# Performance work log

Measured on AMD Instinct MI355X. Metric: run time of the kernel, lower is better.

Reference implementation:

```python
import jax, jax.numpy as jnp
import numpy as np

B, P, S, D, H, DFF, VOC = 8, 16, 512, 512, 8, 2048, 10000
DEPTH = D // H
SIGMA = 0.1
T = 256
LN_EPS = 1e-6


def setup_inputs() -> dict:
    key = jax.random.key(0)
    ks = jax.random.split(key, 40)
    n = lambda i, sh, sc=1.0: jax.random.normal(ks[i], sh, jnp.float32) * sc
    inp = {
        "r": n(0, (B, P, D)),
        "x": jax.random.randint(ks[1], (B, 1), 0, VOC),
        "K": n(2, (B, P, S, D)),
        "Vs": n(3, (B, P, S, D)),
        "w": jax.random.uniform(ks[4], (B, P, 1), jnp.float32),
        "I": jax.random.randint(ks[5], (B, P, S), 0, P),
        "t": T,
        "eps_q": n(6, (B, P, 1, D)),
        "eps_k": n(7, (B, P, 1, D)),
        "eps_v": n(8, (B, P, 1, D)),
        "eps_z": n(9, (B, P, 1, D)),
        "gumbel": -jnp.log(-jnp.log(jax.random.uniform(ks[10], (B, P, P), jnp.float32, 1e-8, 1.0))),
        "Wq": n(11, (D, D), 0.02), "bq": jnp.zeros((D,), jnp.float32),
        "Wk": n(12, (D, D), 0.02), "bk": jnp.zeros((D,), jnp.float32),
        "Wv": n(13, (D, D), 0.02), "bv": jnp.zeros((D,), jnp.float32),
        "Wo": n(14, (D, D), 0.02), "bo": jnp.zeros((D,), jnp.float32),
        "ln1_g": jnp.ones((D,), jnp.float32), "ln1_b": jnp.zeros((D,), jnp.float32),
        "ln3_g": jnp.ones((D,), jnp.float32), "ln3_b": jnp.zeros((D,), jnp.float32),
        "W1": n(15, (D, DFF), 0.02), "b1": jnp.zeros((DFF,), jnp.float32),
        "W2": n(16, (DFF, D), 0.02), "b2": jnp.zeros((D,), jnp.float32),
        "Wout": n(17, (D, VOC), 0.02), "bout": jnp.zeros((VOC,), jnp.float32),
    }
    return inp


def _layernorm(x, g, b):
    mu = jnp.mean(x, axis=-1, keepdims=True)
    var = jnp.mean((x - mu) ** 2, axis=-1, keepdims=True)
    return (x - mu) / jnp.sqrt(var + LN_EPS) * g + b


def _split_heads(x):  # (B,P,L,D) -> (B,P,H,L,depth)
    b, p, l, _ = x.shape
    return x.reshape(b, p, l, H, DEPTH).transpose(0, 1, 3, 2, 4)


def _resample(params, i_t, t):  # reorder particle axis on prefix [:t+1]
    pref = jnp.take_along_axis(params[:, :, :t + 1], i_t[:, :, None, None], axis=1)
    return jnp.concatenate([pref, params[:, :, t + 1:]], axis=2)


def reference(r, x, K, Vs, w, I, t, eps_q, eps_k, eps_v, eps_z, gumbel,
              Wq, bq, Wk, bk, Wv, bv, Wo, bo, ln1_g, ln1_b, ln3_g, ln3_b,
              W1, b1, W2, b2, Wout, bout):
    x = x.astype(jnp.int32)
    I = I.astype(jnp.int32)
    r4 = r[:, :, None, :]                                   # (B,P,1,D)
    # --- mha_smc: noisy projections + K/V buffer update at t ---
    q = r4 @ Wq + bq + SIGMA * eps_q
    k = r4 @ Wk + bk + SIGMA * eps_k
    v = r4 @ Wv + bv + SIGMA * eps_v
    K = K.at[:, :, t, :].set(k[:, :, 0, :])
    Vs = Vs.at[:, :, t, :].set(v[:, :, 0, :])
    qh = _split_heads(q)                                    # (B,P,H,1,depth)
    Kh = _split_heads(K)                                    # (B,P,H,S,depth)
    Vh = _split_heads(Vs)
    scores = jnp.einsum('bphqd,bphsd->bphqs', qh, Kh) / jnp.sqrt(jnp.float32(DEPTH))
    mask = (jnp.arange(S) <= t)[None, None, None, None, :]
    scores = jnp.where(mask, scores, jnp.float32(-1e9))
    attn = jax.nn.softmax(scores, axis=-1)                  # (B,P,H,1,S)
    zh = jnp.einsum('bphqs,bphsd->bphqd', attn, Vh)
    z = zh.transpose(0, 1, 3, 2, 4).reshape(B, P, 1, D) @ Wo + bo
    z = z + SIGMA * eps_z                                   # reparametrized output noise
    attn_weights = jnp.mean(attn, axis=2)                   # (B,P,1,S)
    # --- residual + FFN (dropout disabled: training=False) ---
    out1 = _layernorm(z + r4, ln1_g, ln1_b)
    ffn = jnp.maximum(out1 @ W1 + b1, 0.0) @ W2 + b2
    r_ = _layernorm(ffn + out1, ln3_g, ln3_b)
    predictions = r_ @ Wout + bout                          # (B,P,1,VOC)
    # --- classification importance weights ---
    probs = jax.nn.softmax(predictions, axis=-1)
    idx = jnp.broadcast_to(x.reshape(B, 1, 1, 1), (B, P, 1, 1))
    w_sq = jnp.take_along_axis(probs, idx, axis=-1)[:, :, 0, 0]  # (B,P)
    w_sq = jax.lax.stop_gradient(w_sq)
    pred2 = predictions[:, :, 0, :]                         # (B,P,VOC)
    w_for_pred = w_sq[:, :, None]
    good_avg_pred = jnp.mean(pred2, axis=1, keepdims=True)  # (B,1,VOC)
    avg_pred_after_softmax = jnp.mean(jax.nn.softmax(pred2, axis=-1), axis=1, keepdims=True)
    argmax_w = jnp.argmax(w_for_pred, axis=1)               # (B,1)
    max_prediction = jnp.take_along_axis(pred2, argmax_w[:, :, None], axis=1)  # (B,1,VOC)
    # --- sample_and_keep_indices: Gumbel-max categorical over particles ---
    logits = jnp.log(w_sq + 1e-10)                          # (B,P)
    i_t = jnp.argmax(logits[:, None, :] + gumbel, axis=-1).astype(jnp.int32)  # (B,P)
    I_pref = jnp.take_along_axis(I[:, :, :t], i_t[:, :, None], axis=1)
    I_new = jnp.concatenate([I_pref, i_t[:, :, None], I[:, :, t + 1:]], axis=2)
    # --- resampling (faithful to original: V resampled from already-resampled K) ---
    K = _resample(K, i_t, t)
    Vs = _resample(K, i_t, t)
    z = jnp.take_along_axis(z, I_new[:, :, t][:, :, None, None], axis=1)
    w_new = w_sq[:, :, None]
    return (r4, z, avg_pred_after_softmax, good_avg_pred, max_prediction,
            eps_z, attn_weights, K, Vs, w_new, I_new)
```

## Files before the change

kernel.cpp:

```cpp
#include <hip/hip_runtime.h>

#define NDFF 2048
#define NVOC 10000
#define SIGMA 0.1f

typedef float f32x4 __attribute__((ext_vector_type(4)));

#define O0 0
#define O1 65536
#define O2 131072
#define O3 211072
#define O4 291072
#define O5 371072
#define O6 436608
#define O7 502144
#define O8 34056576
#define O9 67611008
#define O10 67611136

#define WQ    0
#define WK    65536
#define WV    131072
#define WZH   196608
#define WZ    262144
#define WO1   327680
#define WH1   393216
#define WPRED 720896
#define WMAX  2000896
#define WSUM  2001024
#define WWSQ  2001152
#define WIT   2001280
#define WF2P  2001536
#define WSC   2263680

__global__ __launch_bounds__(512)
void k_qkv(const float* __restrict__ r,
           const float* __restrict__ Wq, const float* __restrict__ bq, const float* __restrict__ eq, float* __restrict__ oq,
           const float* __restrict__ Wk, const float* __restrict__ bk, const float* __restrict__ ek, float* __restrict__ ok,
           const float* __restrict__ Wv, const float* __restrict__ bv, const float* __restrict__ ev, float* __restrict__ ov)
{
    const float *W, *bias, *eps; float* out;
    if (blockIdx.z == 0)      { W = Wq; bias = bq; eps = eq; out = oq; }
    else if (blockIdx.z == 1) { W = Wk; bias = bk; eps = ek; out = ok; }
    else                      { W = Wv; bias = bv; eps = ev; out = ov; }
    int tid = threadIdx.x;
    int col = tid & 63, kq = tid >> 6;
    int colg = blockIdx.x * 64 + col;
    int row0 = blockIdx.y * 8;
    __shared__ float rs[8][512];
#pragma unroll
    for (int j = 0; j < 8; j++) rs[j][tid & 511] = r[(row0 + j) * 512 + tid];
    __syncthreads();
    float acc[8] = {0,0,0,0,0,0,0,0};
    const float* Wp = W + (kq * 64) * 512 + colg;
#pragma unroll 8
    for (int d = 0; d < 64; d++) {
        float wv = Wp[d * 512];
#pragma unroll
        for (int p = 0; p < 8; p++) acc[p] += rs[p][kq * 64 + d] * wv;
    }
    __syncthreads();
    float (*part)[8][64] = (float(*)[8][64])rs;
#pragma unroll
    for (int p = 0; p < 8; p++) part[kq][p][col] = acc[p];
    __syncthreads();
    {
        int p = tid >> 6, c = tid & 63;
        int cg = blockIdx.x * 64 + c;
        float v = 0.f;
#pragma unroll
        for (int k = 0; k < 8; k++) v += part[k][p][c];
        out[(row0 + p) * 512 + cg] = v + bias[cg] + SIGMA * eps[(row0 + p) * 512 + cg];
    }
}

__global__ __launch_bounds__(512)
void k_attn(const float* __restrict__ qws, const float* __restrict__ kws,
            const float* __restrict__ vws, const float* __restrict__ Kin,
            const float* __restrict__ Vin, const int* __restrict__ t_ptr,
            float* __restrict__ zh, float* __restrict__ scw)
{
    int t = *t_ptr;
    int bp = blockIdx.x, h = blockIdx.y;
    int tid = threadIdx.x;
    int wave = tid >> 6, lane = tid & 63;
    __shared__ float sc[512];
    __shared__ float red[8], red2[8];
    __shared__ float part[8][64];

    float4 qv = ((const float4*)(qws + bp * 512 + h * 64))[lane & 15];

    for (int sb = wave * 4; sb <= t; sb += 32) {
        int s = sb + (lane >> 4);
        bool valid = (s <= t);
        int ss = valid ? s : t;
        const float4* kr = (ss == t) ? (const float4*)(kws + bp * 512 + h * 64)
                                     : (const float4*)(Kin + (bp * 512 + ss) * 512 + h * 64);
        float4 kv = kr[lane & 15];
        float p = qv.x * kv.x + qv.y * kv.y + qv.z * kv.z + qv.w * kv.w;
#pragma unroll
        for (int m = 1; m < 16; m <<= 1) p += __shfl_xor(p, m, 64);
        if ((lane & 15) == 0 && valid) sc[s] = p * 0.125f;
    }
    __syncthreads();

    float lm = -3.0e38f;
    for (int s = tid; s <= t; s += 512) lm = fmaxf(lm, sc[s]);
#pragma unroll
    for (int o = 32; o; o >>= 1) lm = fmaxf(lm, __shfl_xor(lm, o, 64));
    if (lane == 0) red[wave] = lm;
    __syncthreads();
    float m = red[0];
#pragma unroll
    for (int i = 1; i < 8; i++) m = fmaxf(m, red[i]);
    float ls = 0.f;
    for (int s = tid; s <= t; s += 512) ls += __expf(sc[s] - m);
#pragma unroll
    for (int o = 32; o; o >>= 1) ls += __shfl_xor(ls, o, 64);
    if (lane == 0) red2[wave] = ls;
    __syncthreads();
    float tot = 0.f;
#pragma unroll
    for (int i = 0; i < 8; i++) tot += red2[i];
    float inv = 1.f / tot;
    for (int s = tid; s <= t; s += 512) {
        float a = __expf(sc[s] - m) * inv;
        sc[s] = a;
        scw[(bp * 8 + h) * 512 + s] = a;
    }
    __syncthreads();

    float acc = 0.f;
    const float* Vp = Vin + (bp * 512) * 512 + h * 64 + lane;
    int s = wave;
    for (; s + 24 < t; s += 32) {
        float v0 = __builtin_nontemporal_load(Vp + (size_t)(s     ) * 512);
        float v1 = __builtin_nontemporal_load(Vp + (size_t)(s +  8) * 512);
        float v2 = __builtin_nontemporal_load(Vp + (size_t)(s + 16) * 512);
        float v3 = __builtin_nontemporal_load(Vp + (size_t)(s + 24) * 512);
        acc += sc[s] * v0 + sc[s + 8] * v1 + sc[s + 16] * v2 + sc[s + 24] * v3;
    }
    for (; s < t; s += 8) acc += sc[s] * __builtin_nontemporal_load(Vp + (size_t)s * 512);
    if ((t & 7) == wave) acc += sc[t] * vws[bp * 512 + h * 64 + lane];
    part[wave][lane] = acc;
    __syncthreads();
    if (tid < 64) {
        float v = 0.f;
#pragma unroll
        for (int k = 0; k < 8; k++) v += part[k][tid];
        zh[bp * 512 + h * 64 + tid] = v;
    }
}

__global__ __launch_bounds__(512)
void k_zproj(const float* __restrict__ zh, const float* __restrict__ Wo,
             const float* __restrict__ bo, const float* __restrict__ epsz,
             float* __restrict__ out)
{
    int tid = threadIdx.x;
    int col = tid & 63, kq = tid >> 6;
    int colg = blockIdx.x * 64 + col;
    int row0 = blockIdx.y * 8;
    __shared__ float rs[8][512];
#pragma unroll
    for (int j = 0; j < 8; j++) rs[j][tid] = zh[(row0 + j) * 512 + tid];
    __syncthreads();
    float acc[8] = {0,0,0,0,0,0,0,0};
    const float* Wp = Wo + (kq * 64) * 512 + colg;
#pragma unroll 8
    for (int d = 0; d < 64; d++) {
        float wv = Wp[d * 512];
#pragma unroll
        for (int p = 0; p < 8; p++) acc[p] += rs[p][kq * 64 + d] * wv;
    }
    __syncthreads();
    float (*part)[8][64] = (float(*)[8][64])rs;
#pragma unroll
    for (int p = 0; p < 8; p++) part[kq][p][col] = acc[p];
    __syncthreads();
    {
        int p = tid >> 6, c = tid & 63;
        int cg = blockIdx.x * 64 + c;
        float v = 0.f;
#pragma unroll
        for (int k = 0; k < 8; k++) v += part[k][p][c];
        out[(row0 + p) * 512 + cg] = v + bo[cg] + SIGMA * epsz[(row0 + p) * 512 + cg];
    }
}

__global__ __launch_bounds__(512)
void k_ffn1(const float* __restrict__ zp, const float* __restrict__ r,
            const float* __restrict__ g, const float* __restrict__ be,
            const float* __restrict__ W1, const float* __restrict__ b1,
            float* __restrict__ o1, float* __restrict__ h1)
{
    int tid = threadIdx.x;
    int col = tid & 63, kq = tid >> 6;
    int colg = blockIdx.x * 64 + col;
    int row0 = blockIdx.y * 8;
    __shared__ float rs[8][512];
    __shared__ float sm[8], si[8];
    int wave = tid >> 6, lane = tid & 63;
#pragma unroll
    for (int j = 0; j < 8; j++) {
        int gi = (row0 + j) * 512 + tid;
        rs[j][tid] = zp[gi] + r[gi];
    }
    __syncthreads();
    {
        float s = 0.f;
        for (int c = lane; c < 512; c += 64) s += rs[wave][c];
#pragma unroll
        for (int o = 32; o; o >>= 1) s += __shfl_xor(s, o, 64);
        float mu = s * (1.f / 512.f);
        float v = 0.f;
        for (int c = lane; c < 512; c += 64) { float dx = rs[wave][c] - mu; v += dx * dx; }
#pragma unroll
        for (int o = 32; o; o >>= 1) v += __shfl_xor(v, o, 64);
        if (lane == 0) { sm[wave] = mu; si[wave] = rsqrtf(v * (1.f / 512.f) + 1e-6f); }
    }
    __syncthreads();
#pragma unroll
    for (int j = 0; j < 8; j++) {
        float val = (rs[j][tid] - sm[j]) * si[j] * g[tid] + be[tid];
        rs[j][tid] = val;
        if (blockIdx.x == 0) o1[(row0 + j) * 512 + tid] = val;
    }
    __syncthreads();
    float acc[8] = {0,0,0,0,0,0,0,0};
    const float* Wp = W1 + (kq * 64) * NDFF + colg;
#pragma unroll 8
    for (int d = 0; d < 64; d++) {
        float wv = Wp[d * NDFF];
#pragma unroll
        for (int p = 0; p < 8; p++) acc[p] += rs[p][kq * 64 + d] * wv;
    }
    __syncthreads();
    float (*part)[8][64] = (float(*)[8][64])rs;
#pragma unroll
    for (int p = 0; p < 8; p++) part[kq][p][col] = acc[p];
    __syncthreads();
    {
        int p = tid >> 6, c = tid & 63;
        int cg = blockIdx.x * 64 + c;
        float v = 0.f;
#pragma unroll
        for (int k = 0; k < 8; k++) v += part[k][p][c];
        h1[(row0 + p) * NDFF + cg] = fmaxf(v + b1[cg], 0.f);
    }
}

__global__ __launch_bounds__(512)
void k_ffn2p(const float* __restrict__ h1, const float* __restrict__ W2,
             float* __restrict__ f2p)
{
    int tid = threadIdx.x;
    int col = tid & 63, kq = tid >> 6;
    int colg = blockIdx.x * 64 + col;
    int row0 = blockIdx.y * 8;
    int ks = blockIdx.z;
    __shared__ float rs[8][512];
#pragma unroll
    for (int j = 0; j < 8; j++)
        rs[j][tid] = h1[(row0 + j) * NDFF + ks * 512 + tid];
    __syncthreads();
    float acc[8] = {0,0,0,0,0,0,0,0};
    const float* Wp = W2 + (ks * 512 + kq * 64) * 512 + colg;
#pragma unroll 8
    for (int d = 0; d < 64; d++) {
        float wv = Wp[d * 512];
#pragma unroll
        for (int p = 0; p < 8; p++) acc[p] += rs[p][kq * 64 + d] * wv;
    }
    __syncthreads();
    float (*part)[8][64] = (float(*)[8][64])rs;
#pragma unroll
    for (int p = 0; p < 8; p++) part[kq][p][col] = acc[p];
    __syncthreads();
    {
        int p = tid >> 6, c = tid & 63;
        int cg = blockIdx.x * 64 + c;
        float v = 0.f;
#pragma unroll
        for (int k = 0; k < 8; k++) v += part[k][p][c];
        f2p[ks * 65536 + (row0 + p) * 512 + cg] = v;
    }
}

__global__ __launch_bounds__(512)
void k_pred(const float* __restrict__ f2p, const float* __restrict__ b2,
            const float* __restrict__ o1, const float* __restrict__ g3,
            const float* __restrict__ b3, const float* __restrict__ Wout,
            const float* __restrict__ bout, float* __restrict__ pred)
{
    int tid = threadIdx.x;
    int col = tid & 255, kh = tid >> 8;
    int colg = blockIdx.x * 256 + col;
    int colL = min(colg, NVOC - 1);
    int row0 = blockIdx.y * 16;
    __shared__ float rs[16][512];
    __shared__ float sm[16], si[16];
    int wave = tid >> 6, lane = tid & 63;
#pragma unroll
    for (int j = 0; j < 16; j++) {
        int gi = (row0 + j) * 512 + tid;
        rs[j][tid] = f2p[gi] + f2p[65536 + gi] + f2p[131072 + gi] + f2p[196608 + gi]
                   + b2[tid] + o1[gi];
    }
    __syncthreads();
    {
        int row = wave * 2 + (lane >> 5);
        int l = lane & 31;
        float s = 0.f;
        for (int c = l; c < 512; c += 32) s += rs[row][c];
#pragma unroll
        for (int o = 16; o; o >>= 1) s += __shfl_xor(s, o, 64);
        float mu = s * (1.f / 512.f);
        float v = 0.f;
        for (int c = l; c < 512; c += 32) { float dx = rs[row][c] - mu; v += dx * dx; }
#pragma unroll
        for (int o = 16; o; o >>= 1) v += __shfl_xor(v, o, 64);
        if (l == 0) { sm[row] = mu; si[row] = rsqrtf(v * (1.f / 512.f) + 1e-6f); }
    }
    __syncthreads();
#pragma unroll
    for (int j = 0; j < 16; j++)
        rs[j][tid] = (rs[j][tid] - sm[j]) * si[j] * g3[tid] + b3[tid];
    __syncthreads();
    float acc[16];
#pragma unroll
    for (int p = 0; p < 16; p++) acc[p] = 0.f;
    const float* Wp = Wout + (kh * 256) * NVOC + colL;
#pragma unroll 4
    for (int d = 0; d < 256; d++) {
        float wv = Wp[d * NVOC];
#pragma unroll
        for (int p = 0; p < 16; p++) acc[p] += rs[p][kh * 256 + d] * wv;
    }
    __syncthreads();
    float (*part)[256] = (float(*)[256])rs;
    if (kh == 1) {
#pragma unroll
        for (int p = 0; p < 16; p++) part[p][col] = acc[p];
    }
    __syncthreads();
    if (kh == 0 && colg < NVOC) {
        float bv = bout[colg];
#pragma unroll
        for (int p = 0; p < 16; p++)
            pred[(row0 + p) * NVOC + colg] = acc[p] + part[p][col] + bv;
    }
}

__global__ __launch_bounds__(512)
void k_soft(const float* __restrict__ pred, const int* __restrict__ x,
            const float* __restrict__ scw, const int* __restrict__ t_ptr,
            float* __restrict__ rowmax, float* __restrict__ rowsum,
            float* __restrict__ wsq, float* __restrict__ out)
{
    __shared__ float red[8];
    int row = blockIdx.x, tid = threadIdx.x;
    {
        int t = *t_ptr;
        float a = 0.f;
        if (tid <= t) {
#pragma unroll
            for (int hh = 0; hh < 8; hh++) a += scw[(row * 8 + hh) * 512 + tid];
            a *= 0.125f;
        }
        out[O6 + row * 512 + tid] = a;
    }
    const float* pr = pred + row * NVOC;
    float m = -3.0e38f;
    for (int v = tid; v < NVOC; v += 512) m = fmaxf(m, pr[v]);
#pragma unroll
    for (int o = 32; o; o >>= 1) m = fmaxf(m, __shfl_xor(m, o, 64));
    if ((tid & 63) == 0) red[tid >> 6] = m;
    __syncthreads();
#pragma unroll
    for (int i = 0; i < 8; i++) m = fmaxf(m, red[i]);
    __syncthreads();
    float s = 0.f;
    for (int v = tid; v < NVOC; v += 512) s += __expf(pr[v] - m);
#pragma unroll
    for (int o = 32; o; o >>= 1) s += __shfl_xor(s, o, 64);
    if ((tid & 63) == 0) red[tid >> 6] = s;
    __syncthreads();
    if (tid == 0) {
        float tot = 0.f;
#pragma unroll
        for (int i = 0; i < 8; i++) tot += red[i];
        rowmax[row] = m; rowsum[row] = tot;
        int b = row >> 4;
        float w = __expf(pr[x[b]] - m) / tot;
        wsq[row] = w;
        out[O9 + row] = w;
    }
}

__global__ __launch_bounds__(512)
void k_vocab(const float* __restrict__ pred, const float* __restrict__ rowmax,
             const float* __restrict__ rowsum, const float* __restrict__ wsq,
             const float* __restrict__ gumbel, int* __restrict__ it,
             float* __restrict__ out)
{
    int b = blockIdx.y;
    int tid = threadIdx.x;
    __shared__ int s_amw;
    if (tid == 0) {
        float bw = -3.0e38f; int bj = 0;
#pragma unroll
        for (int pp = 0; pp < 16; pp++) {
            float wv = wsq[b * 16 + pp];
            if (wv > bw) { bw = wv; bj = pp; }
        }
        s_amw = bj;
    }
    if (blockIdx.x == 0 && tid < 16) {
        float best = -3.0e38f; int bi = 0;
#pragma unroll
        for (int pp = 0; pp < 16; pp++) {
            float v = logf(wsq[b * 16 + pp] + 1e-10f) + gumbel[(b * 16 + tid) * 16 + pp];
            if (v > best) { best = v; bi = pp; }
        }
        it[b * 16 + tid] = bi;
    }
    __syncthreads();
    int v = blockIdx.x * 512 + tid;
    if (v >= NVOC) return;
    int amw = s_amw;
    float ga = 0.f, as = 0.f;
#pragma unroll
    for (int p = 0; p < 16; p++) {
        int rr = b * 16 + p;
        float pv = pred[rr * NVOC + v];
        ga += pv;
        as += __expf(pv - rowmax[rr]) * (1.f / rowsum[rr]);
    }
    out[O3 + b * NVOC + v] = ga * (1.f / 16.f);
    out[O2 + b * NVOC + v] = as * (1.f / 16.f);
    out[O4 + b * NVOC + v] = pred[(b * 16 + amw) * NVOC + v];
}

__global__ __launch_bounds__(256)
void k_resample(const float* __restrict__ Kin, const float* __restrict__ kws,
                const int* __restrict__ it, const int* __restrict__ t_ptr,
                const float* __restrict__ r, const float* __restrict__ epsz,
                const float* __restrict__ zws, const int* __restrict__ Iin,
                float* __restrict__ out)
{
    int t = *t_ptr;
    const f32x4* K4  = (const f32x4*)Kin;
    const f32x4* kw4 = (const f32x4*)kws;
    const f32x4* r4  = (const f32x4*)r;
    const f32x4* e4  = (const f32x4*)epsz;
    const f32x4* z4  = (const f32x4*)zws;
    f32x4* oK = (f32x4*)(out + O7);
    f32x4* oV = (f32x4*)(out + O8);
    const int total = 128 * 512 * 128;
    const int total2 = total + 16384;
    for (int i = blockIdx.x * 256 + threadIdx.x; i < total2; i += gridDim.x * 256) {
        if (i < total) {
            int lane = i & 127;
            int row = i >> 7;
            int s = row & 511;
            int bp = row >> 9;
            int b = bp >> 4;
            f32x4 vK, vV;
            if (s > t) {
                vK = __builtin_nontemporal_load(&K4[i]);
                vV = vK;
            } else {
                int ip = it[bp];
                int ip2 = it[b * 16 + ip];
                if (s == t) {
                    vK = kw4[(b * 16 + ip) * 128 + lane];
                    vV = kw4[(b * 16 + ip2) * 128 + lane];
                } else {
                    vK = K4[((b * 16 + ip) * 512 + s) * 128 + lane];
                    vV = K4[((b * 16 + ip2) * 512 + s) * 128 + lane];
                }
            }
            __builtin_nontemporal_store(vK, &oK[i]);
            __builtin_nontemporal_store(vV, &oV[i]);
        } else {
            int j = i - total;
            int fidx = j * 4;
            ((f32x4*)(out + O0))[j] = r4[j];
            ((f32x4*)(out + O5))[j] = e4[j];
            int row = fidx >> 9, d0 = fidx & 511;
            int b = row >> 4;
            int ip = it[row];
            ((f32x4*)(out + O1))[j] = z4[((b * 16 + ip) << 7) + (d0 >> 2)];
#pragma unroll
            for (int k = 0; k < 4; k++) {
                int s = d0 + k;
                float iv;
                if (s < t)       iv = (float)Iin[((b * 16 + ip) << 9) + s];
                else if (s == t) iv = (float)ip;
                else             iv = (float)Iin[row * 512 + s];
                out[O10 + fidx + k] = iv;
            }
        }
    }
}

extern "C" void kernel_launch(void* const* d_in, const int* in_sizes, int n_in,
                              void* d_out, int out_size, void* d_ws, size_t ws_size,
                              hipStream_t stream) {
    const float* r      = (const float*)d_in[0];
    const int*   x      = (const int*)d_in[1];
    const float* Kin    = (const float*)d_in[2];
    const float* Vin    = (const float*)d_in[3];
    const int*   Iin    = (const int*)d_in[5];
    const int*   t_ptr  = (const int*)d_in[6];
    const float* eps_q  = (const float*)d_in[7];
    const float* eps_k  = (const float*)d_in[8];
    const float* eps_v  = (const float*)d_in[9];
    const float* eps_z  = (const float*)d_in[10];
    const float* gumbel = (const float*)d_in[11];
    const float* Wq = (const float*)d_in[12]; const float* bq = (const float*)d_in[13];
    const float* Wk = (const float*)d_in[14]; const float* bk = (const float*)d_in[15];
    const float* Wv = (const float*)d_in[16]; const float* bv = (const float*)d_in[17];
    const float* Wo = (const float*)d_in[18]; const float* bo = (const float*)d_in[19];
    const float* ln1_g = (const float*)d_in[20]; const float* ln1_b = (const float*)d_in[21];
    const float* ln3_g = (const float*)d_in[22]; const float* ln3_b = (const float*)d_in[23];
    const float* W1 = (const float*)d_in[24]; const float* b1 = (const float*)d_in[25];
    const float* W2 = (const float*)d_in[26]; const float* b2 = (const float*)d_in[27];
    const float* Wout = (const float*)d_in[28]; const float* bout = (const float*)d_in[29];

    float* ws  = (float*)d_ws;
    float* q   = ws + WQ;
    float* kv  = ws + WK;
    float* vv  = ws + WV;
    float* zh  = ws + WZH;
    float* zp  = ws + WZ;
    float* o1  = ws + WO1;
    float* h1  = ws + WH1;
    float* pr  = ws + WPRED;
    float* rmx = ws + WMAX;
    float* rsm = ws + WSUM;
    float* wsq = ws + WWSQ;
    int*   itw = (int*)(ws + WIT);
    float* f2p = ws + WF2P;
    float* scw = ws + WSC;
    float* outp = (float*)d_out;

    k_qkv<<<dim3(8, 16, 3), 512, 0, stream>>>(r, Wq, bq, eps_q, q, Wk, bk, eps_k, kv, Wv, bv, eps_v, vv);
    k_attn<<<dim3(128, 8), 512, 0, stream>>>(q, kv, vv, Kin, Vin, t_ptr, zh, scw);
    k_zproj<<<dim3(8, 16), 512, 0, stream>>>(zh, Wo, bo, eps_z, zp);
    k_ffn1<<<dim3(32, 16), 512, 0, stream>>>(zp, r, ln1_g, ln1_b, W1, b1, o1, h1);
    k_ffn2p<<<dim3(8, 16, 4), 512, 0, stream>>>(h1, W2, f2p);
    k_pred<<<dim3(40, 8), 512, 0, stream>>>(f2p, b2, o1, ln3_g, ln3_b, Wout, bout, pr);
    k_soft<<<128, 512, 0, stream>>>(pr, x, scw, t_ptr, rmx, rsm, wsq, outp);
    k_vocab<<<dim3(20, 8), 512, 0, stream>>>(pr, rmx, rsm, wsq, gumbel, itw, outp);
    k_resample<<<4096, 256, 0, stream>>>(Kin, kv, itw, t_ptr, r, eps_z, zp, Iin, outp);
}
```

Measured before the change: 199.5 us.

## Overlap K/V tail copy with small GEMM kernels via extra copy blocks

```diff
diff --git a/kernel.cpp b/kernel.cpp
--- a/kernel.cpp
+++ b/kernel.cpp
@@ -33,6 +33,28 @@
 #define WF2P  2001536
 #define WSC   2263680
 
+__device__ __forceinline__ void copy_sgt(const float* __restrict__ Kin,
+                                         float* __restrict__ out, int t,
+                                         int q, int bid, int nblk, int tid, int nthr)
+{
+    const f32x4* K4 = (const f32x4*)Kin;
+    f32x4* oK = (f32x4*)(out + O7);
+    f32x4* oV = (f32x4*)(out + O8);
+    int cnt = 511 - t;
+    long totalc = (long)128 * cnt * 128;
+    long q0 = (totalc * q) >> 2, q1 = (totalc * (q + 1)) >> 2;
+    for (long j = q0 + (long)bid * nthr + tid; j < q1; j += (long)nblk * nthr) {
+        int lane = (int)(j & 127);
+        long row = j >> 7;
+        int bp = (int)(row / cnt);
+        int s = t + 1 + (int)(row - (long)bp * cnt);
+        long i = ((long)(bp * 512 + s) << 7) + lane;
+        f32x4 v = __builtin_nontemporal_load(&K4[i]);
+        __builtin_nontemporal_store(v, &oK[i]);
+        __builtin_nontemporal_store(v, &oV[i]);
+    }
+}
+
 __global__ __launch_bounds__(512)
 void k_qkv(const float* __restrict__ r,
            const float* __restrict__ Wq, const float* __restrict__ bq, const float* __restrict__ eq, float* __restrict__ oq,
@@ -155,8 +177,14 @@
 __global__ __launch_bounds__(512)
 void k_zproj(const float* __restrict__ zh, const float* __restrict__ Wo,
              const float* __restrict__ bo, const float* __restrict__ epsz,
-             float* __restrict__ out)
-{
+             const float* __restrict__ Kin, const int* __restrict__ t_ptr,
+             float* __restrict__ outbuf, float* __restrict__ out)
+{
+    if (blockIdx.x >= 8) {
+        int bid = (blockIdx.x - 8) * 16 + blockIdx.y;
+        copy_sgt(Kin, outbuf, *t_ptr, 0, bid, 64, threadIdx.x, 512);
+        return;
+    }
     int tid = threadIdx.x;
     int col = tid & 63, kq = tid >> 6;
     int colg = blockIdx.x * 64 + col;
@@ -192,8 +220,15 @@
 void k_ffn1(const float* __restrict__ zp, const float* __restrict__ r,
             const float* __restrict__ g, const float* __restrict__ be,
             const float* __restrict__ W1, const float* __restrict__ b1,
+            const float* __restrict__ Kin, const int* __restrict__ t_ptr,
+            float* __restrict__ outbuf,
             float* __restrict__ o1, float* __restrict__ h1)
 {
+    if (blockIdx.x >= 32) {
+        int bid = (blockIdx.x - 32) * 16 + blockIdx.y;
+        copy_sgt(Kin, outbuf, *t_ptr, 1, bid, 64, threadIdx.x, 512);
+        return;
+    }
     int tid = threadIdx.x;
     int col = tid & 63, kq = tid >> 6;
     int colg = blockIdx.x * 64 + col;
@@ -252,8 +287,14 @@
 
 __global__ __launch_bounds__(512)
 void k_ffn2p(const float* __restrict__ h1, const float* __restrict__ W2,
-             float* __restrict__ f2p)
-{
+             const float* __restrict__ Kin, const int* __restrict__ t_ptr,
+             float* __restrict__ outbuf, float* __restrict__ f2p)
+{
+    if (blockIdx.x >= 8) {
+        int bid = blockIdx.y * 4 + blockIdx.z;
+        copy_sgt(Kin, outbuf, *t_ptr, 2, bid, 64, threadIdx.x, 512);
+        return;
+    }
     int tid = threadIdx.x;
     int col = tid & 63, kq = tid >> 6;
     int colg = blockIdx.x * 64 + col;
@@ -291,8 +332,15 @@
 void k_pred(const float* __restrict__ f2p, const float* __restrict__ b2,
             const float* __restrict__ o1, const float* __restrict__ g3,
             const float* __restrict__ b3, const float* __restrict__ Wout,
-            const float* __restrict__ bout, float* __restrict__ pred)
-{
+            const float* __restrict__ bout,
+            const float* __restrict__ Kin, const int* __restrict__ t_ptr,
+            float* __restrict__ outbuf, float* __restrict__ pred)
+{
+    if (blockIdx.x >= 40) {
+        int bid = (blockIdx.x - 40) * 8 + blockIdx.y;
+        copy_sgt(Kin, outbuf, *t_ptr, 3, bid, 64, threadIdx.x, 512);
+        return;
+    }
     int tid = threadIdx.x;
     int col = tid & 255, kh = tid >> 8;
     int colg = blockIdx.x * 256 + col;
@@ -457,41 +505,38 @@
     const f32x4* z4  = (const f32x4*)zws;
     f32x4* oK = (f32x4*)(out + O7);
     f32x4* oV = (f32x4*)(out + O8);
-    const int total = 128 * 512 * 128;
-    const int total2 = total + 16384;
-    for (int i = blockIdx.x * 256 + threadIdx.x; i < total2; i += gridDim.x * 256) {
-        if (i < total) {
-            int lane = i & 127;
-            int row = i >> 7;
-            int s = row & 511;
-            int bp = row >> 9;
+    int cnt = t + 1;
+    long total = (long)128 * cnt * 128;
+    long total2 = total + 16384;
+    for (long j = (long)blockIdx.x * 256 + threadIdx.x; j < total2; j += (long)gridDim.x * 256) {
+        if (j < total) {
+            int lane = (int)(j & 127);
+            long row = j >> 7;
+            int bp = (int)(row / cnt);
+            int s = (int)(row - (long)bp * cnt);
             int b = bp >> 4;
+            int ip = it[bp];
+            int ip2 = it[b * 16 + ip];
             f32x4 vK, vV;
-            if (s > t) {
-                vK = __builtin_nontemporal_load(&K4[i]);
-                vV = vK;
+            if (s == t) {
+                vK = kw4[(b * 16 + ip) * 128 + lane];
+                vV = kw4[(b * 16 + ip2) * 128 + lane];
             } else {
-                int ip = it[bp];
-                int ip2 = it[b * 16 + ip];
-                if (s == t) {
-                    vK = kw4[(b * 16 + ip) * 128 + lane];
-                    vV = kw4[(b * 16 + ip2) * 128 + lane];
-                } else {
-                    vK = K4[((b * 16 + ip) * 512 + s) * 128 + lane];
-                    vV = K4[((b * 16 + ip2) * 512 + s) * 128 + lane];
-                }
+                vK = K4[((long)((b * 16 + ip) * 512 + s) << 7) + lane];
+                vV = K4[((long)((b * 16 + ip2) * 512 + s) << 7) + lane];
             }
+            long i = ((long)(bp * 512 + s) << 7) + lane;
             __builtin_nontemporal_store(vK, &oK[i]);
             __builtin_nontemporal_store(vV, &oV[i]);
         } else {
-            int j = i - total;
-            int fidx = j * 4;
-            ((f32x4*)(out + O0))[j] = r4[j];
-            ((f32x4*)(out + O5))[j] = e4[j];
+            int jj = (int)(j - total);
+            int fidx = jj * 4;
+            ((f32x4*)(out + O0))[jj] = r4[jj];
+            ((f32x4*)(out + O5))[jj] = e4[jj];
             int row = fidx >> 9, d0 = fidx & 511;
             int b = row >> 4;
             int ip = it[row];
-            ((f32x4*)(out + O1))[j] = z4[((b * 16 + ip) << 7) + (d0 >> 2)];
+            ((f32x4*)(out + O1))[jj] = z4[((b * 16 + ip) << 7) + (d0 >> 2)];
 #pragma unroll
             for (int k = 0; k < 4; k++) {
                 int s = d0 + k;
@@ -548,11 +593,11 @@
 
     k_qkv<<<dim3(8, 16, 3), 512, 0, stream>>>(r, Wq, bq, eps_q, q, Wk, bk, eps_k, kv, Wv, bv, eps_v, vv);
     k_attn<<<dim3(128, 8), 512, 0, stream>>>(q, kv, vv, Kin, Vin, t_ptr, zh, scw);
-    k_zproj<<<dim3(8, 16), 512, 0, stream>>>(zh, Wo, bo, eps_z, zp);
-    k_ffn1<<<dim3(32, 16), 512, 0, stream>>>(zp, r, ln1_g, ln1_b, W1, b1, o1, h1);
-    k_ffn2p<<<dim3(8, 16, 4), 512, 0, stream>>>(h1, W2, f2p);
-    k_pred<<<dim3(40, 8), 512, 0, stream>>>(f2p, b2, o1, ln3_g, ln3_b, Wout, bout, pr);
+    k_zproj<<<dim3(12, 16), 512, 0, stream>>>(zh, Wo, bo, eps_z, Kin, t_ptr, outp, zp);
+    k_ffn1<<<dim3(36, 16), 512, 0, stream>>>(zp, r, ln1_g, ln1_b, W1, b1, Kin, t_ptr, outp, o1, h1);
+    k_ffn2p<<<dim3(9, 16, 4), 512, 0, stream>>>(h1, W2, Kin, t_ptr, outp, f2p);
+    k_pred<<<dim3(48, 8), 512, 0, stream>>>(f2p, b2, o1, ln3_g, ln3_b, Wout, bout, Kin, t_ptr, outp, pr);
     k_soft<<<128, 512, 0, stream>>>(pr, x, scw, t_ptr, rmx, rsm, wsq, outp);
     k_vocab<<<dim3(20, 8), 512, 0, stream>>>(pr, rmx, rsm, wsq, gumbel, itw, outp);
-    k_resample<<<4096, 256, 0, stream>>>(Kin, kv, itw, t_ptr, r, eps_z, zp, Iin, outp);
-}
+    k_resample<<<2048, 256, 0, stream>>>(Kin, kv, itw, t_ptr, r, eps_z, zp, Iin, outp);
+}
```

After: 232.6 us. 1.17x slower.
